# Optimization experiments

Hardware: AMD Instinct MI355X
Metric: run time of the kernel (lower is better)

Reference implementation:

```python
import jax, jax.numpy as jnp
import numpy as np

THRESHOLD = 0.5

# Per face-direction (z-, z+, y-, y+, x-, x+), the 4 quad-vertex grid offsets
# (dz, dy, dx) where a coordinate c-0.5 maps to grid index c and c+0.5 to c+1.
# Order matches the original torch code's v0..v3 exactly.
QUAD_OFFS = np.array([
    [[0,0,0],[0,0,1],[0,1,0],[0,1,1]],  # z- face
    [[1,0,0],[1,0,1],[1,1,0],[1,1,1]],  # z+ face
    [[1,0,0],[1,0,1],[0,0,0],[0,0,1]],  # y- face
    [[0,1,0],[0,1,1],[1,1,0],[1,1,1]],  # y+ face
    [[1,0,0],[0,0,0],[1,1,0],[0,1,0]],  # x- face
    [[0,0,1],[1,0,1],[0,1,1],[1,1,1]],  # x+ face
], dtype=np.int32)
# Each quad -> 2 triangles: (v0,v1,v2), (v1,v2,v3)
TRI_SEL = np.array([[0,1,2],[1,2,3]], dtype=np.int32)
FACE_OFFS = QUAD_OFFS[:, TRI_SEL, :]  # [6, 2, 3, 3]


def setup_inputs() -> dict:
    key = jax.random.key(0)
    voxel_probas = jax.random.uniform(key, (4, 32, 32, 32), dtype=jnp.float32)
    return {"voxel_probas": voxel_probas}


def reference(voxel_probas):
    thr = THRESHOLD
    N, C, H, W = voxel_probas.shape
    occ = voxel_probas > thr
    pad = jnp.pad(occ, ((0, 0), (1, 1), (1, 1), (1, 1)))  # boundary = unoccupied
    # neighbor occupancy in the 6 directions (z-, z+, y-, y+, x-, x+)
    nb = jnp.stack([
        pad[:, :-2, 1:-1, 1:-1], pad[:, 2:, 1:-1, 1:-1],
        pad[:, 1:-1, :-2, 1:-1], pad[:, 1:-1, 2:, 1:-1],
        pad[:, 1:-1, 1:-1, :-2], pad[:, 1:-1, 1:-1, 2:],
    ], axis=-1)  # [N,C,H,W,6]
    exposed = occ[..., None] & ~nb  # face emitted iff voxel occupied & neighbor empty

    # canonical grid vertex ids (replaces python dict dedup; vertices live on a
    # (C+1)x(H+1)x(W+1) half-integer grid)
    zz, yy, xx = jnp.meshgrid(jnp.arange(C), jnp.arange(H), jnp.arange(W), indexing='ij')
    base = jnp.stack([zz, yy, xx], axis=-1)  # [C,H,W,3]
    gc = base[:, :, :, None, None, None, :] + jnp.asarray(FACE_OFFS)[None, None, None]  # [C,H,W,6,2,3,3]
    vid_local = (gc[..., 0] * (H + 1) + gc[..., 1]) * (W + 1) + gc[..., 2]  # [C,H,W,6,2,3]
    Vg = (C + 1) * (H + 1) * (W + 1)
    batch_off = (jnp.arange(N, dtype=jnp.int32) * Vg).reshape(N, 1, 1, 1, 1, 1, 1)
    faces = (vid_local[None].astype(jnp.int32) + batch_off).reshape(-1, 3)  # [Fmax,3]
    face_mask = jnp.repeat(exposed[..., None], 2, axis=-1).reshape(-1)       # [Fmax]

    # full grid vertex positions per sample (z-0.5, y-0.5, x-0.5 style coords)
    gz, gy, gx = jnp.meshgrid(jnp.arange(C + 1), jnp.arange(H + 1), jnp.arange(W + 1), indexing='ij')
    grid_pos = jnp.stack([gz, gy, gx], axis=-1).reshape(-1, 3).astype(jnp.float32) - 0.5
    vertex_positions = jnp.tile(grid_pos, (N, 1))  # [N*Vg,3]

    # which grid vertices are actually referenced by a valid face
    used = (jnp.zeros(N * Vg, jnp.int32)
            .at[faces.reshape(-1)]
            .add(jnp.repeat(face_mask.astype(jnp.int32), 3)) > 0)
    vpos_masked = jnp.where(used[:, None], vertex_positions, 0.0)

    # undirected edge index, same construction/order as the original:
    # (v0,v1) for all faces, then (v1,v2), then (v0,v2), then all reversed
    fwd_edges = jnp.concatenate([faces[:, [0, 1]], faces[:, [1, 2]], faces[:, [0, 2]]], axis=0)
    edge_index = jnp.concatenate([fwd_edges, fwd_edges[:, ::-1]], axis=0).T  # [2, 6*Fmax]
    edge_mask = jnp.tile(face_mask, 6)

    vert_counts = used.reshape(N, Vg).sum(-1)
    face_counts = face_mask.reshape(N, -1).sum(-1)
    return (vert_counts, face_counts, vpos_masked, used, edge_index, faces, face_mask, edge_mask)
```

## Files before the change

kernel.cpp:

```cpp
#include <hip/hip_runtime.h>

#define VG     35937
#define NVOX   131072
#define NPAIR  393216
#define NF4    393216

#define O_VC   0
#define O_FC   4
#define O_VP   8
#define O_US   431252
#define O_EI   575000
#define O_FA   19449368
#define O_FM   24167960
#define O_EM   25740824

#define NQB    1536
#define BPB    141
#define NVB    (4 * BPB)

__global__ __launch_bounds__(256) void cubify_fused(
    const float* __restrict__ probas, float* __restrict__ out) {
  __shared__ int wsum[4];
  int lane = threadIdx.x & 63, wid = threadIdx.x >> 6;
  int b = blockIdx.x;

  if (b < NQB) {
    int t = b * 256 + threadIdx.x;
    int v = t / 3;
    int fp = t - 3 * v;
    int x = v & 31, y = (v >> 5) & 31, z = (v >> 10) & 31, n = v >> 15;

    float m0 = 0.0f, m1 = 0.0f;
    if (probas[v] > 0.5f) {
      bool nm, np;
      if (fp == 0)      { nm = (z > 0)  && probas[v - 1024] > 0.5f;
                          np = (z < 31) && probas[v + 1024] > 0.5f; }
      else if (fp == 1) { nm = (y > 0)  && probas[v - 32]   > 0.5f;
                          np = (y < 31) && probas[v + 32]   > 0.5f; }
      else              { nm = (x > 0)  && probas[v - 1]    > 0.5f;
                          np = (x < 31) && probas[v + 1]    > 0.5f; }
      m0 = nm ? 0.0f : 1.0f;
      m1 = np ? 0.0f : 1.0f;
    }

    int base = n * VG + (z * 33 + y) * 33 + x;
    float c0 = (float)(base);        float c1 = (float)(base + 1);
    float c2 = (float)(base + 33);   float c3 = (float)(base + 34);
    float c4 = (float)(base + 1089); float c5 = (float)(base + 1090);
    float c6 = (float)(base + 1122); float c7 = (float)(base + 1123);

    float a0, a1, a2, a3, b0, b1, b2, b3;
    if (fp == 0)      { a0=c0; a1=c1; a2=c2; a3=c3;  b0=c4; b1=c5; b2=c6; b3=c7; }
    else if (fp == 1) { a0=c4; a1=c5; a2=c0; a3=c1;  b0=c2; b1=c3; b2=c6; b3=c7; }
    else              { a0=c4; a1=c0; a2=c6; a3=c2;  b0=c1; b1=c5; b2=c3; b3=c7; }

    float4 M  = make_float4(m0, m0, m1, m1);
    float4 A  = make_float4(a0, a1, b0, b1);
    float4 B  = make_float4(a1, a2, b1, b2);
    float4 Cc = make_float4(a2, a3, b2, b3);

    ((float4*)(out + O_FM))[t] = M;

    float4* em = (float4*)(out + O_EM);
    #pragma unroll
    for (int j = 0; j < 6; ++j) em[j * NF4 + t] = M;

    float4* ei = (float4*)(out + O_EI);
    ei[ 0 * NF4 + t] = A;  ei[ 1 * NF4 + t] = B;  ei[ 2 * NF4 + t] = A;
    ei[ 3 * NF4 + t] = B;  ei[ 4 * NF4 + t] = Cc; ei[ 5 * NF4 + t] = Cc;
    ei[ 6 * NF4 + t] = B;  ei[ 7 * NF4 + t] = Cc; ei[ 8 * NF4 + t] = Cc;
    ei[ 9 * NF4 + t] = A;  ei[10 * NF4 + t] = B;  ei[11 * NF4 + t] = A;

    float4* fa = (float4*)(out + O_FA + 12 * t);
    fa[0] = make_float4(a0, a1, a2, a1);
    fa[1] = make_float4(a2, a3, b0, b1);
    fa[2] = make_float4(b2, b1, b2, b3);

    int cnt = 2 * ((m0 > 0.0f) + (m1 > 0.0f));
    for (int d = 32; d > 0; d >>= 1) cnt += __shfl_down(cnt, d, 64);
    if (lane == 0) wsum[wid] = cnt;
    __syncthreads();
    if (threadIdx.x == 0)
      atomicAdd(&out[O_FC + n], (float)(wsum[0] + wsum[1] + wsum[2] + wsum[3]));
  } else {
    int b2 = b - NQB;
    int n  = b2 / BPB;
    int li = (b2 - n * BPB) * 256 + threadIdx.x;
    int u = 0;
    if (li < VG) {
      int gz = li / 1089;
      int r  = li - gz * 1089;
      int gy = r / 33;
      int gx = r - gy * 33;
      bool any_occ = false, all_occ = true;
      #pragma unroll
      for (int dz = 0; dz < 2; ++dz)
        #pragma unroll
        for (int dy = 0; dy < 2; ++dy)
          #pragma unroll
          for (int dx = 0; dx < 2; ++dx) {
            int z = gz - dz, y = gy - dy, x = gx - dx;
            if (z >= 0 && z < 32 && y >= 0 && y < 32 && x >= 0 && x < 32) {
              bool o = probas[((n * 32 + z) * 32 + y) * 32 + x] > 0.5f;
              any_occ |= o; all_occ &= o;
            } else {
              all_occ = false;
            }
          }
      u = (any_occ && !all_occ) ? 1 : 0;

      int idx = n * VG + li;
      out[O_US + idx] = u ? 1.0f : 0.0f;
      float* vp = out + O_VP + 3 * idx;
      if (u) {
        vp[0] = (float)gz - 0.5f;
        vp[1] = (float)gy - 0.5f;
        vp[2] = (float)gx - 0.5f;
      } else {
        vp[0] = 0.0f; vp[1] = 0.0f; vp[2] = 0.0f;
      }
    }
    int cnt = u;
    for (int d = 32; d > 0; d >>= 1) cnt += __shfl_down(cnt, d, 64);
    if (lane == 0) wsum[wid] = cnt;
    __syncthreads();
    if (threadIdx.x == 0)
      atomicAdd(&out[O_VC + n], (float)(wsum[0] + wsum[1] + wsum[2] + wsum[3]));
  }
}

extern "C" void kernel_launch(void* const* d_in, const int* in_sizes, int n_in,
                              void* d_out, int out_size, void* d_ws, size_t ws_size,
                              hipStream_t stream) {
  const float* probas = (const float*)d_in[0];
  float* out = (float*)d_out;
  cubify_fused<<<NQB + NVB, 256, 0, stream>>>(probas, out);
}
```

Measured before the change: 150.9 us.

## Use nontemporal stores and LDS-transposed coalesced face writes

All large output writes now use nontemporal vector stores so the streaming output bypasses or deprioritizes cache retention. The faces output, previously written as three strided float4 stores per thread (48-byte stride), is staged through shared memory and written back so consecutive threads store consecutive float4s. This costs 12 KB of LDS per block and extra shared-memory traffic with integer index math, which could lower occupancy.

```diff
diff --git a/kernel.cpp b/kernel.cpp
--- a/kernel.cpp
+++ b/kernel.cpp
@@ -18,14 +18,22 @@
 #define BPB    141
 #define NVB    (4 * BPB)
 
+typedef float f4 __attribute__((ext_vector_type(4)));
+
+__device__ __forceinline__ void ntst(float* p, f4 v) {
+  __builtin_nontemporal_store(v, (f4*)p);
+}
+
 __global__ __launch_bounds__(256) void cubify_fused(
     const float* __restrict__ probas, float* __restrict__ out) {
+  __shared__ float lfac[12 * 256];
   __shared__ int wsum[4];
-  int lane = threadIdx.x & 63, wid = threadIdx.x >> 6;
+  int tid = threadIdx.x;
+  int lane = tid & 63, wid = tid >> 6;
   int b = blockIdx.x;
 
   if (b < NQB) {
-    int t = b * 256 + threadIdx.x;
+    int t = b * 256 + tid;
     int v = t / 3;
     int fp = t - 3 * v;
     int x = v & 31, y = (v >> 5) & 31, z = (v >> 10) & 31, n = v >> 15;
@@ -54,38 +62,57 @@
     else if (fp == 1) { a0=c4; a1=c5; a2=c0; a3=c1;  b0=c2; b1=c3; b2=c6; b3=c7; }
     else              { a0=c4; a1=c0; a2=c6; a3=c2;  b0=c1; b1=c5; b2=c3; b3=c7; }
 
-    float4 M  = make_float4(m0, m0, m1, m1);
-    float4 A  = make_float4(a0, a1, b0, b1);
-    float4 B  = make_float4(a1, a2, b1, b2);
-    float4 Cc = make_float4(a2, a3, b2, b3);
+    f4 M  = {m0, m0, m1, m1};
+    f4 A  = {a0, a1, b0, b1};
+    f4 B  = {a1, a2, b1, b2};
+    f4 Cc = {a2, a3, b2, b3};
 
-    ((float4*)(out + O_FM))[t] = M;
+    ntst(out + O_FM + 4 * t, M);
 
-    float4* em = (float4*)(out + O_EM);
     #pragma unroll
-    for (int j = 0; j < 6; ++j) em[j * NF4 + t] = M;
+    for (int j = 0; j < 6; ++j) ntst(out + O_EM + 4 * (j * NF4 + t), M);
 
-    float4* ei = (float4*)(out + O_EI);
-    ei[ 0 * NF4 + t] = A;  ei[ 1 * NF4 + t] = B;  ei[ 2 * NF4 + t] = A;
-    ei[ 3 * NF4 + t] = B;  ei[ 4 * NF4 + t] = Cc; ei[ 5 * NF4 + t] = Cc;
-    ei[ 6 * NF4 + t] = B;  ei[ 7 * NF4 + t] = Cc; ei[ 8 * NF4 + t] = Cc;
-    ei[ 9 * NF4 + t] = A;  ei[10 * NF4 + t] = B;  ei[11 * NF4 + t] = A;
+    float* ei = out + O_EI;
+    ntst(ei + 4 * ( 0 * NF4 + t), A);  ntst(ei + 4 * ( 1 * NF4 + t), B);
+    ntst(ei + 4 * ( 2 * NF4 + t), A);  ntst(ei + 4 * ( 3 * NF4 + t), B);
+    ntst(ei + 4 * ( 4 * NF4 + t), Cc); ntst(ei + 4 * ( 5 * NF4 + t), Cc);
+    ntst(ei + 4 * ( 6 * NF4 + t), B);  ntst(ei + 4 * ( 7 * NF4 + t), Cc);
+    ntst(ei + 4 * ( 8 * NF4 + t), Cc); ntst(ei + 4 * ( 9 * NF4 + t), A);
+    ntst(ei + 4 * (10 * NF4 + t), B);  ntst(ei + 4 * (11 * NF4 + t), A);
 
-    float4* fa = (float4*)(out + O_FA + 12 * t);
-    fa[0] = make_float4(a0, a1, a2, a1);
-    fa[1] = make_float4(a2, a3, b0, b1);
-    fa[2] = make_float4(b2, b1, b2, b3);
+    lfac[ 0 * 256 + tid] = a0;  lfac[ 1 * 256 + tid] = a1;
+    lfac[ 2 * 256 + tid] = a2;  lfac[ 3 * 256 + tid] = a1;
+    lfac[ 4 * 256 + tid] = a2;  lfac[ 5 * 256 + tid] = a3;
+    lfac[ 6 * 256 + tid] = b0;  lfac[ 7 * 256 + tid] = b1;
+    lfac[ 8 * 256 + tid] = b2;  lfac[ 9 * 256 + tid] = b1;
+    lfac[10 * 256 + tid] = b2;  lfac[11 * 256 + tid] = b3;
 
     int cnt = 2 * ((m0 > 0.0f) + (m1 > 0.0f));
     for (int d = 32; d > 0; d >>= 1) cnt += __shfl_down(cnt, d, 64);
     if (lane == 0) wsum[wid] = cnt;
     __syncthreads();
-    if (threadIdx.x == 0)
+
+    float* fa = out + O_FA + b * 3072;
+    #pragma unroll
+    for (int r = 0; r < 3; ++r) {
+      int p = tid + 256 * r;
+      f4 val;
+      #pragma unroll
+      for (int k = 0; k < 4; ++k) {
+        int q = 4 * p + k;
+        int lt = q / 12;
+        int jj = q - lt * 12;
+        val[k] = lfac[jj * 256 + lt];
+      }
+      ntst(fa + 4 * p, val);
+    }
+
+    if (tid == 0)
       atomicAdd(&out[O_FC + n], (float)(wsum[0] + wsum[1] + wsum[2] + wsum[3]));
   } else {
     int b2 = b - NQB;
     int n  = b2 / BPB;
-    int li = (b2 - n * BPB) * 256 + threadIdx.x;
+    int li = (b2 - n * BPB) * 256 + tid;
     int u = 0;
     if (li < VG) {
       int gz = li / 1089;
```

New measurement: 160.4 us. +6.4%, slower.
